# Performance work log

Hardware: AMD Instinct MI355X
Metric: run time of the kernel (lower is better)

## Reference

```python
import math
import jax, jax.numpy as jnp
import numpy as np

B, N, D, H = 4, 2048, 512, 8
HD = D // H


def setup_inputs() -> dict:
    key = jax.random.key(0)
    ks = jax.random.split(key, 7)
    w_scale = 1.0 / math.sqrt(D)  # keep logits in a sane range (like default init)
    return {
        "q": jax.random.normal(ks[0], (B, N, D), dtype=jnp.float32),
        "mask": jax.random.randint(ks[1], (B, N), 0, 2) == 1,  # True = masked key
        "attn_bias": jax.random.normal(ks[2], (B, N, N), dtype=jnp.float32),
        "Wq": jax.random.normal(ks[3], (D, D), dtype=jnp.float32) * w_scale,
        "Wk": jax.random.normal(ks[4], (D, D), dtype=jnp.float32) * w_scale,
        "Wv": jax.random.normal(ks[5], (D, D), dtype=jnp.float32) * w_scale,
        "Wo": jax.random.normal(ks[6], (D, D), dtype=jnp.float32) * w_scale,
    }


def _heads(v):
    # [B, N, D] -> [H, B, N, HD]  (mirrors reshape + movedim(-2, 0))
    b, n, d = v.shape
    return v.reshape(b, n, H, HD).transpose(2, 0, 1, 3)


def reference(q, mask, attn_bias, Wq, Wk, Wv, Wo):
    # Linear projections (torch Linear: x @ W.T)
    qh = _heads(q @ Wq.T)
    kh = _heads(q @ Wk.T)   # self-attention: h defaults to q
    vh = _heads(q @ Wv.T)
    # scores: [H, B, Nq, Nk]
    scores = jnp.einsum("hbqd,hbkd->hbqk", qh, kh) / math.sqrt(HD)
    scores = scores + attn_bias[None]                     # broadcast over heads
    scores = jnp.where(mask[None, :, None, :], -jnp.inf, scores)
    attn = jax.nn.softmax(scores, axis=-1)
    out = jnp.einsum("hbqk,hbkd->hbqd", attn, vh)         # [H, B, Nq, HD]
    out = out.transpose(1, 2, 0, 3).reshape(q.shape[0], q.shape[1], D)
    return out @ Wo.T
```

## Files before the change

kernel.cpp:

```cpp
#include <hip/hip_runtime.h>
#include <stdint.h>


typedef __attribute__((ext_vector_type(8))) short short8;
typedef __attribute__((ext_vector_type(4))) short short4v;
typedef __attribute__((ext_vector_type(4))) float f32x4;

#define DEV static __device__ __forceinline__

constexpr int Bc = 4, Nc = 2048, Dc = 512, Hc = 8, HDc = 64;
constexpr int Mc = Bc * Nc;
constexpr int QKVNc = 3 * Dc;

DEV unsigned short f2bits(float f) {
  union { float f; unsigned u; } a; a.f = f;
  unsigned r = a.u + 0x7fffu + ((a.u >> 16) & 1u);
  return (unsigned short)(r >> 16);
}
DEV unsigned pack_bf16x2(float a, float b) {
  unsigned ua = __float_as_uint(a), ub = __float_as_uint(b);
  ua = ua + 0x7fffu + ((ua >> 16) & 1u);
  ub = ub + 0x7fffu + ((ub >> 16) & 1u);
  return __builtin_amdgcn_perm(ub, ua, 0x07060302);
}
DEV unsigned pack_shorts(short a, short b) {
  return (unsigned)(unsigned short)a | ((unsigned)(unsigned short)b << 16);
}
DEV short8 cvt8(float4 a, float4 b) {
  union { short8 s; uint4 u; } r;
  r.u.x = pack_bf16x2(a.x, a.y); r.u.y = pack_bf16x2(a.z, a.w);
  r.u.z = pack_bf16x2(b.x, b.y); r.u.w = pack_bf16x2(b.z, b.w);
  return r.s;
}

__global__ void cvtw_kernel(const float* __restrict__ Wq, const float* __restrict__ Wk,
                            const float* __restrict__ Wv, const float* __restrict__ Wo,
                            short* __restrict__ Wqkv, short* __restrict__ Wob) {
  int which = blockIdx.x >> 8;
  int j = (blockIdx.x & 255) * 256 + threadIdx.x;
  const float* src = which == 0 ? Wq : which == 1 ? Wk : which == 2 ? Wv : Wo;
  short* dst = (which == 3) ? Wob : Wqkv + which * (Dc * Dc);
  float4 v = ((const float4*)src)[j];
  short4v o = { (short)f2bits(v.x), (short)f2bits(v.y), (short)f2bits(v.z), (short)f2bits(v.w) };
  ((short4v*)dst)[j] = o;
}

__global__ void maskprep_kernel(const void* __restrict__ mask, float* __restrict__ mf) {
  __shared__ int flag;
  if (threadIdx.x == 0) flag = 0;
  __syncthreads();
  const uchar4* m4 = (const uchar4*)mask;
  int acc = 0;
  for (int i = threadIdx.x; i < 2048; i += 1024) {
    uchar4 v = m4[i];
    acc |= (int)v.y | (int)v.z | (int)v.w;
  }
  if (acc) atomicOr(&flag, 1);
  __syncthreads();
  int isbyte = flag;
  for (int i = threadIdx.x; i < Bc * Nc; i += 1024) {
    int v = isbyte ? (int)((const unsigned char*)mask)[i] : ((const int*)mask)[i];
    mf[i] = v ? -1e30f : 0.0f;
  }
}

template<bool A_F32, bool OUT_F32>
__global__ __launch_bounds__(256, 2) void gemm_bt(const void* __restrict__ Av,
                                                  const short* __restrict__ Bm,
                                                  void* __restrict__ Cv,
                                                  int M, int N, int K,
                                                  int qcols, float cscale) {
  __shared__ __align__(16) short At[128 * 72];
  __shared__ __align__(16) short Bt[128 * 72];
  const int tid = threadIdx.x, lane = tid & 63, wv = tid >> 6;
  const int quad = lane >> 4, l16 = lane & 15;
  const int mbase = blockIdx.y * 128, nbase = blockIdx.x * 128;
  const int wr = (wv >> 1) * 64, wc = (wv & 1) * 64;
  const float scale = (nbase < qcols) ? cscale : 1.0f;
  f32x4 acc[4][4] = {};
  float4 apf[4][2]; short8 aph[4], bpre[4];
#pragma unroll
  for (int i = 0; i < 4; i++) {
    int flat = i * 256 + tid, row = flat >> 3, ch8 = (flat & 7) * 8;
    if (A_F32) {
      const float* Af = (const float*)Av;
      apf[i][0] = *(const float4*)&Af[(size_t)(mbase + row) * K + ch8];
      apf[i][1] = *(const float4*)&Af[(size_t)(mbase + row) * K + ch8 + 4];
    } else {
      aph[i] = *(const short8*)&((const short*)Av)[(size_t)(mbase + row) * K + ch8];
    }
    bpre[i] = *(const short8*)&Bm[(size_t)(nbase + row) * K + ch8];
  }
  for (int k0 = 0; k0 < K; k0 += 64) {
    __syncthreads();
#pragma unroll
    for (int i = 0; i < 4; i++) {
      int flat = i * 256 + tid, row = flat >> 3, ch8 = (flat & 7) * 8;
      *(short8*)&At[row * 72 + ch8] = A_F32 ? cvt8(apf[i][0], apf[i][1]) : aph[i];
      *(short8*)&Bt[row * 72 + ch8] = bpre[i];
    }
    if (k0 + 64 < K) {
#pragma unroll
      for (int i = 0; i < 4; i++) {
        int flat = i * 256 + tid, row = flat >> 3, ch8 = (flat & 7) * 8;
        if (A_F32) {
          const float* Af = (const float*)Av;
          apf[i][0] = *(const float4*)&Af[(size_t)(mbase + row) * K + k0 + 64 + ch8];
          apf[i][1] = *(const float4*)&Af[(size_t)(mbase + row) * K + k0 + 64 + ch8 + 4];
        } else {
          aph[i] = *(const short8*)&((const short*)Av)[(size_t)(mbase + row) * K + k0 + 64 + ch8];
        }
        bpre[i] = *(const short8*)&Bm[(size_t)(nbase + row) * K + k0 + 64 + ch8];
      }
    }
    __syncthreads();
#pragma unroll
    for (int s = 0; s < 2; s++) {
      short8 af[4], bf[4];
#pragma unroll
      for (int t = 0; t < 4; t++) {
        af[t] = *(short8*)&At[(wr + t * 16 + l16) * 72 + quad * 8 + s * 32];
        bf[t] = *(short8*)&Bt[(wc + t * 16 + l16) * 72 + quad * 8 + s * 32];
      }
#pragma unroll
      for (int mt = 0; mt < 4; mt++)
#pragma unroll
        for (int nt = 0; nt < 4; nt++)
          acc[mt][nt] = __builtin_amdgcn_mfma_f32_16x16x32_bf16(af[mt], bf[nt], acc[mt][nt], 0, 0, 0);
    }
  }
#pragma unroll
  for (int mt = 0; mt < 4; mt++)
#pragma unroll
    for (int nt = 0; nt < 4; nt++)
#pragma unroll
      for (int r = 0; r < 4; r++) {
        int row = mbase + wr + mt * 16 + quad * 4 + r;
        int col = nbase + wc + nt * 16 + l16;
        float v = acc[mt][nt][r] * scale;
        if (OUT_F32) ((float*)Cv)[(size_t)row * N + col] = v;
        else         ((short*)Cv)[(size_t)row * N + col] = (short)f2bits(v);
      }
}

__global__ __launch_bounds__(512, 3) void attn_kernel(const short* __restrict__ QKV,
                                                      const float* __restrict__ bias,
                                                      const float* __restrict__ maskf,
                                                      short* __restrict__ Aout) {
  __shared__ __align__(16) short Kt[64 * 72];
  __shared__ __align__(16) short Vt[64 * 72];
  __shared__ __align__(16) short Pt[8][16 * 72];
  __shared__ __align__(16) float mlds[Nc];
  __shared__ float lred[8][16];
  const int tid = threadIdx.x, lane = tid & 63, wv = tid >> 6;
  const int quad = lane >> 4, l16 = lane & 15;
  const int qt = blockIdx.x & 15, h = (blockIdx.x >> 4) & 7, b = (int)(blockIdx.x >> 7);
  const int qrow0 = qt * 128;
  const int qglob = qrow0 + wv * 16 + l16;
  const float* biasrow = bias + ((size_t)b * Nc + qglob) * Nc;
  const float* mfb = maskf + b * Nc;

  ((float4*)mlds)[tid] = ((const float4*)mfb)[tid];

  short8 qf[2];
  {
    const short* qp = QKV + (size_t)(b * Nc + qglob) * QKVNc + h * HDc + quad * 8;
    qf[0] = *(const short8*)qp;
    qf[1] = *(const short8*)(qp + 32);
  }

  const int vp = tid & 31, vq = tid >> 5;
  const int krow = tid >> 3, kch = (tid & 7) * 8;
  const short* Kbase = QKV + Dc + h * HDc;
  const short* Vbase = QKV + 2 * Dc + h * HDc;

  short8 kpre; short4v v0pre, v1pre; float4 bpre[4];
  kpre  = *(const short8*)&Kbase[(size_t)(b * Nc + krow) * QKVNc + kch];
  v0pre = *(const short4v*)&Vbase[(size_t)(b * Nc + 2 * vp) * QKVNc + 4 * vq];
  v1pre = *(const short4v*)&Vbase[(size_t)(b * Nc + 2 * vp + 1) * QKVNc + 4 * vq];
#pragma unroll
  for (int t = 0; t < 4; t++) bpre[t] = *(const float4*)&biasrow[t * 16 + quad * 4];

  f32x4 oacc[4] = {};
  float lsum = 0.f;

  for (int kt = 0; kt < 32; kt++) {
    const int kb = kt * 64;
    const int kbn = ((kt + 1) & 31) * 64;
    __syncthreads();
    *(short8*)&Kt[krow * 72 + kch] = kpre;
#pragma unroll
    for (int j = 0; j < 4; j++)
      *(unsigned*)&Vt[(4 * vq + j) * 72 + 2 * vp] = pack_shorts(v0pre[j], v1pre[j]);

    float4 bcur[4];
#pragma unroll
    for (int t = 0; t < 4; t++) bcur[t] = bpre[t];
    kpre  = *(const short8*)&Kbase[(size_t)(b * Nc + kbn + krow) * QKVNc + kch];
    v0pre = *(const short4v*)&Vbase[(size_t)(b * Nc + kbn + 2 * vp) * QKVNc + 4 * vq];
    v1pre = *(const short4v*)&Vbase[(size_t)(b * Nc + kbn + 2 * vp + 1) * QKVNc + 4 * vq];
#pragma unroll
    for (int t = 0; t < 4; t++) bpre[t] = *(const float4*)&biasrow[kbn + t * 16 + quad * 4];
    __syncthreads();

    f32x4 sacc[4] = {};
#pragma unroll
    for (int s = 0; s < 2; s++)
#pragma unroll
      for (int t = 0; t < 4; t++) {
        short8 kf = *(short8*)&Kt[(t * 16 + l16) * 72 + quad * 8 + s * 32];
        sacc[t] = __builtin_amdgcn_mfma_f32_16x16x32_bf16(kf, qf[s], sacc[t], 0, 0, 0);
      }

#pragma unroll
    for (int t = 0; t < 4; t++) {
      float4 mv = *(const float4*)&mlds[kb + t * 16 + quad * 4];
      float p0 = __expf(sacc[t][0] + mv.x + bcur[t].x);
      float p1 = __expf(sacc[t][1] + mv.y + bcur[t].y);
      float p2 = __expf(sacc[t][2] + mv.z + bcur[t].z);
      float p3 = __expf(sacc[t][3] + mv.w + bcur[t].w);
      lsum += (p0 + p1) + (p2 + p3);
      uint2 u = { pack_bf16x2(p0, p1), pack_bf16x2(p2, p3) };
      *(uint2*)&Pt[wv][l16 * 72 + t * 16 + quad * 4] = u;
    }

#pragma unroll
    for (int s = 0; s < 2; s++) {
      short8 pf = *(short8*)&Pt[wv][l16 * 72 + quad * 8 + s * 32];
#pragma unroll
      for (int t = 0; t < 4; t++) {
        short8 vf = *(short8*)&Vt[(t * 16 + l16) * 72 + quad * 8 + s * 32];
        oacc[t] = __builtin_amdgcn_mfma_f32_16x16x32_bf16(pf, vf, oacc[t], 0, 0, 0);
      }
    }
  }

  lsum += __shfl_xor(lsum, 16);
  lsum += __shfl_xor(lsum, 32);
  if (quad == 0) lred[wv][l16] = lsum;
#pragma unroll
  for (int r = 0; r < 4; r++) {
    float inv = 1.0f / lred[wv][quad * 4 + r];
    int row = b * Nc + qrow0 + wv * 16 + quad * 4 + r;
#pragma unroll
    for (int t = 0; t < 4; t++)
      Aout[(size_t)row * Dc + h * HDc + t * 16 + l16] = (short)f2bits(oacc[t][r] * inv);
  }
}

extern "C" void kernel_launch(void* const* d_in, const int* in_sizes, int n_in,
                              void* d_out, int out_size, void* d_ws, size_t ws_size,
                              hipStream_t stream) {
  const float* q    = (const float*)d_in[0];
  const void*  mask = d_in[1];
  const float* bias = (const float*)d_in[2];
  const float* Wq   = (const float*)d_in[3];
  const float* Wk   = (const float*)d_in[4];
  const float* Wv   = (const float*)d_in[5];
  const float* Wo   = (const float*)d_in[6];
  float* out = (float*)d_out;

  char* ws = (char*)d_ws;
  short* Wqkv = (short*)ws;  ws += (size_t)QKVNc * Dc * 2;
  short* Wob  = (short*)ws;  ws += (size_t)Dc * Dc * 2;
  float* mf   = (float*)ws;  ws += (size_t)Bc * Nc * 4;
  short* QKV  = (short*)ws;  ws += (size_t)Mc * QKVNc * 2;
  short* aout = (short*)ws;  ws += (size_t)Mc * Dc * 2;

  cvtw_kernel<<<dim3(1024), dim3(256), 0, stream>>>(Wq, Wk, Wv, Wo, Wqkv, Wob);
  maskprep_kernel<<<dim3(1), dim3(1024), 0, stream>>>(mask, mf);

  gemm_bt<true, false><<<dim3(QKVNc / 128, Mc / 128), dim3(256), 0, stream>>>(
      (const void*)q, Wqkv, (void*)QKV, Mc, QKVNc, Dc, Dc, 0.125f);
  attn_kernel<<<dim3(Bc * Hc * 16), dim3(512), 0, stream>>>(QKV, bias, mf, aout);
  gemm_bt<false, true><<<dim3(Dc / 128, Mc / 128), dim3(256), 0, stream>>>(
      (const void*)aout, Wob, (void*)out, Mc, Dc, Dc, 0, 1.0f);
}
```

Baseline: 261.5 us.

## Use exp2 with prefolded log2e, MFMA row sums, smaller attention blocks

The attention kernel now runs 256-thread blocks over 64 query rows, giving twice as many blocks. Scores come out pre-scaled by log2(e) and are exponentiated with exp2. The bias and mask are preloaded into the MFMA accumulator so the add is folded into the matmul. Row sums of P are computed with an MFMA against a ones vector, which removes the scalar adds and the shuffle reduction. bf16 conversion switches to the native cast, and the new tiling doubles how often each K/V tile is reloaded into LDS across blocks.

```diff
diff --git a/kernel.cpp b/kernel.cpp
--- a/kernel.cpp
+++ b/kernel.cpp
@@ -11,26 +11,31 @@
 constexpr int Bc = 4, Nc = 2048, Dc = 512, Hc = 8, HDc = 64;
 constexpr int Mc = Bc * Nc;
 constexpr int QKVNc = 3 * Dc;
-
-DEV unsigned short f2bits(float f) {
-  union { float f; unsigned u; } a; a.f = f;
-  unsigned r = a.u + 0x7fffu + ((a.u >> 16) & 1u);
-  return (unsigned short)(r >> 16);
-}
-DEV unsigned pack_bf16x2(float a, float b) {
-  unsigned ua = __float_as_uint(a), ub = __float_as_uint(b);
-  ua = ua + 0x7fffu + ((ua >> 16) & 1u);
-  ub = ub + 0x7fffu + ((ub >> 16) & 1u);
-  return __builtin_amdgcn_perm(ub, ua, 0x07060302);
+constexpr float L2E = 1.44269504f;
+
+DEV short bf16cast(float f) {
+  return (short)__builtin_bit_cast(unsigned short, (__bf16)f);
+}
+DEV unsigned cvt_pk_bf16(float a, float b) {
+  unsigned short lb = __builtin_bit_cast(unsigned short, (__bf16)a);
+  unsigned short hb = __builtin_bit_cast(unsigned short, (__bf16)b);
+  return (unsigned)lb | ((unsigned)hb << 16);
 }
 DEV unsigned pack_shorts(short a, short b) {
   return (unsigned)(unsigned short)a | ((unsigned)(unsigned short)b << 16);
 }
 DEV short8 cvt8(float4 a, float4 b) {
   union { short8 s; uint4 u; } r;
-  r.u.x = pack_bf16x2(a.x, a.y); r.u.y = pack_bf16x2(a.z, a.w);
-  r.u.z = pack_bf16x2(b.x, b.y); r.u.w = pack_bf16x2(b.z, b.w);
+  r.u.x = cvt_pk_bf16(a.x, a.y); r.u.y = cvt_pk_bf16(a.z, a.w);
+  r.u.z = cvt_pk_bf16(b.x, b.y); r.u.w = cvt_pk_bf16(b.z, b.w);
   return r.s;
+}
+DEV float fast_exp2(float x) {
+#if __has_builtin(__builtin_amdgcn_exp2f)
+  return __builtin_amdgcn_exp2f(x);
+#else
+  return exp2f(x);
+#endif
 }
 
 __global__ void cvtw_kernel(const float* __restrict__ Wq, const float* __restrict__ Wk,
@@ -41,7 +46,7 @@
   const float* src = which == 0 ? Wq : which == 1 ? Wk : which == 2 ? Wv : Wo;
   short* dst = (which == 3) ? Wob : Wqkv + which * (Dc * Dc);
   float4 v = ((const float4*)src)[j];
-  short4v o = { (short)f2bits(v.x), (short)f2bits(v.y), (short)f2bits(v.z), (short)f2bits(v.w) };
+  short4v o = { bf16cast(v.x), bf16cast(v.y), bf16cast(v.z), bf16cast(v.w) };
   ((short4v*)dst)[j] = o;
 }
 
@@ -139,28 +144,28 @@
         int col = nbase + wc + nt * 16 + l16;
         float v = acc[mt][nt][r] * scale;
         if (OUT_F32) ((float*)Cv)[(size_t)row * N + col] = v;
-        else         ((short*)Cv)[(size_t)row * N + col] = (short)f2bits(v);
-      }
-}
-
-__global__ __launch_bounds__(512, 3) void attn_kernel(const short* __restrict__ QKV,
+        else         ((short*)Cv)[(size_t)row * N + col] = bf16cast(v);
+      }
+}
+
+__global__ __launch_bounds__(256, 4) void attn_kernel(const short* __restrict__ QKV,
                                                       const float* __restrict__ bias,
                                                       const float* __restrict__ maskf,
                                                       short* __restrict__ Aout) {
   __shared__ __align__(16) short Kt[64 * 72];
   __shared__ __align__(16) short Vt[64 * 72];
-  __shared__ __align__(16) short Pt[8][16 * 72];
+  __shared__ __align__(16) short Pt[4][16 * 72];
   __shared__ __align__(16) float mlds[Nc];
-  __shared__ float lred[8][16];
   const int tid = threadIdx.x, lane = tid & 63, wv = tid >> 6;
   const int quad = lane >> 4, l16 = lane & 15;
-  const int qt = blockIdx.x & 15, h = (blockIdx.x >> 4) & 7, b = (int)(blockIdx.x >> 7);
-  const int qrow0 = qt * 128;
+  const int qt = blockIdx.x & 31, h = (blockIdx.x >> 5) & 7, b = (int)(blockIdx.x >> 8);
+  const int qrow0 = qt * 64;
   const int qglob = qrow0 + wv * 16 + l16;
   const float* biasrow = bias + ((size_t)b * Nc + qglob) * Nc;
   const float* mfb = maskf + b * Nc;
 
-  ((float4*)mlds)[tid] = ((const float4*)mfb)[tid];
+  ((float4*)mlds)[tid]       = ((const float4*)mfb)[tid];
+  ((float4*)mlds)[tid + 256] = ((const float4*)mfb)[tid + 256];
 
   short8 qf[2];
   {
@@ -174,36 +179,56 @@
   const short* Kbase = QKV + Dc + h * HDc;
   const short* Vbase = QKV + 2 * Dc + h * HDc;
 
-  short8 kpre; short4v v0pre, v1pre; float4 bpre[4];
-  kpre  = *(const short8*)&Kbase[(size_t)(b * Nc + krow) * QKVNc + kch];
-  v0pre = *(const short4v*)&Vbase[(size_t)(b * Nc + 2 * vp) * QKVNc + 4 * vq];
-  v1pre = *(const short4v*)&Vbase[(size_t)(b * Nc + 2 * vp + 1) * QKVNc + 4 * vq];
+  short8 kpre0, kpre1; short4v v0pre[2], v1pre[2]; float4 bpre[4];
+  kpre0 = *(const short8*)&Kbase[(size_t)(b * Nc + krow) * QKVNc + kch];
+  kpre1 = *(const short8*)&Kbase[(size_t)(b * Nc + krow + 32) * QKVNc + kch];
+#pragma unroll
+  for (int g = 0; g < 2; g++) {
+    v0pre[g] = *(const short4v*)&Vbase[(size_t)(b * Nc + 2 * vp) * QKVNc + 4 * (vq + 8 * g)];
+    v1pre[g] = *(const short4v*)&Vbase[(size_t)(b * Nc + 2 * vp + 1) * QKVNc + 4 * (vq + 8 * g)];
+  }
 #pragma unroll
   for (int t = 0; t < 4; t++) bpre[t] = *(const float4*)&biasrow[t * 16 + quad * 4];
 
+  const short ONEB = (short)0x3F80;
+  const short8 ones = { ONEB, ONEB, ONEB, ONEB, ONEB, ONEB, ONEB, ONEB };
+
   f32x4 oacc[4] = {};
-  float lsum = 0.f;
+  f32x4 sumacc = {};
 
   for (int kt = 0; kt < 32; kt++) {
     const int kb = kt * 64;
     const int kbn = ((kt + 1) & 31) * 64;
     __syncthreads();
-    *(short8*)&Kt[krow * 72 + kch] = kpre;
-#pragma unroll
-    for (int j = 0; j < 4; j++)
-      *(unsigned*)&Vt[(4 * vq + j) * 72 + 2 * vp] = pack_shorts(v0pre[j], v1pre[j]);
-
-    float4 bcur[4];
-#pragma unroll
-    for (int t = 0; t < 4; t++) bcur[t] = bpre[t];
-    kpre  = *(const short8*)&Kbase[(size_t)(b * Nc + kbn + krow) * QKVNc + kch];
-    v0pre = *(const short4v*)&Vbase[(size_t)(b * Nc + kbn + 2 * vp) * QKVNc + 4 * vq];
-    v1pre = *(const short4v*)&Vbase[(size_t)(b * Nc + kbn + 2 * vp + 1) * QKVNc + 4 * vq];
+    *(short8*)&Kt[krow * 72 + kch] = kpre0;
+    *(short8*)&Kt[(krow + 32) * 72 + kch] = kpre1;
+#pragma unroll
+    for (int g = 0; g < 2; g++)
+#pragma unroll
+      for (int j = 0; j < 4; j++)
+        *(unsigned*)&Vt[(4 * (vq + 8 * g) + j) * 72 + 2 * vp] = pack_shorts(v0pre[g][j], v1pre[g][j]);
+
+    f32x4 sacc[4];
+#pragma unroll
+    for (int t = 0; t < 4; t++) {
+      float4 mv = *(const float4*)&mlds[kb + t * 16 + quad * 4];
+      sacc[t][0] = __builtin_fmaf(bpre[t].x, L2E, mv.x);
+      sacc[t][1] = __builtin_fmaf(bpre[t].y, L2E, mv.y);
+      sacc[t][2] = __builtin_fmaf(bpre[t].z, L2E, mv.z);
+      sacc[t][3] = __builtin_fmaf(bpre[t].w, L2E, mv.w);
+    }
+
+    kpre0 = *(const short8*)&Kbase[(size_t)(b * Nc + kbn + krow) * QKVNc + kch];
+    kpre1 = *(const short8*)&Kbase[(size_t)(b * Nc + kbn + krow + 32) * QKVNc + kch];
+#pragma unroll
+    for (int g = 0; g < 2; g++) {
+      v0pre[g] = *(const short4v*)&Vbase[(size_t)(b * Nc + kbn + 2 * vp) * QKVNc + 4 * (vq + 8 * g)];
+      v1pre[g] = *(const short4v*)&Vbase[(size_t)(b * Nc + kbn + 2 * vp + 1) * QKVNc + 4 * (vq + 8 * g)];
+    }
 #pragma unroll
     for (int t = 0; t < 4; t++) bpre[t] = *(const float4*)&biasrow[kbn + t * 16 + quad * 4];
     __syncthreads();
 
-    f32x4 sacc[4] = {};
 #pragma unroll
     for (int s = 0; s < 2; s++)
 #pragma unroll
@@ -214,19 +239,18 @@
 
 #pragma unroll
     for (int t = 0; t < 4; t++) {
-      float4 mv = *(const float4*)&mlds[kb + t * 16 + quad * 4];
-      float p0 = __expf(sacc[t][0] + mv.x + bcur[t].x);
-      float p1 = __expf(sacc[t][1] + mv.y + bcur[t].y);
-      float p2 = __expf(sacc[t][2] + mv.z + bcur[t].z);
-      float p3 = __expf(sacc[t][3] + mv.w + bcur[t].w);
-      lsum += (p0 + p1) + (p2 + p3);
-      uint2 u = { pack_bf16x2(p0, p1), pack_bf16x2(p2, p3) };
+      float p0 = fast_exp2(sacc[t][0]);
+      float p1 = fast_exp2(sacc[t][1]);
+      float p2 = fast_exp2(sacc[t][2]);
+      float p3 = fast_exp2(sacc[t][3]);
+      uint2 u = { cvt_pk_bf16(p0, p1), cvt_pk_bf16(p2, p3) };
       *(uint2*)&Pt[wv][l16 * 72 + t * 16 + quad * 4] = u;
     }
 
 #pragma unroll
     for (int s = 0; s < 2; s++) {
       short8 pf = *(short8*)&Pt[wv][l16 * 72 + quad * 8 + s * 32];
+      sumacc = __builtin_amdgcn_mfma_f32_16x16x32_bf16(pf, ones, sumacc, 0, 0, 0);
 #pragma unroll
       for (int t = 0; t < 4; t++) {
         short8 vf = *(short8*)&Vt[(t * 16 + l16) * 72 + quad * 8 + s * 32];
@@ -235,16 +259,13 @@
     }
   }
 
-  lsum += __shfl_xor(lsum, 16);
-  lsum += __shfl_xor(lsum, 32);
-  if (quad == 0) lred[wv][l16] = lsum;
 #pragma unroll
   for (int r = 0; r < 4; r++) {
-    float inv = 1.0f / lred[wv][quad * 4 + r];
+    float inv = 1.0f / sumacc[r];
     int row = b * Nc + qrow0 + wv * 16 + quad * 4 + r;
 #pragma unroll
     for (int t = 0; t < 4; t++)
-      Aout[(size_t)row * Dc + h * HDc + t * 16 + l16] = (short)f2bits(oacc[t][r] * inv);
+      Aout[(size_t)row * Dc + h * HDc + t * 16 + l16] = bf16cast(oacc[t][r] * inv);
   }
 }
 
@@ -271,8 +292,8 @@
   maskprep_kernel<<<dim3(1), dim3(1024), 0, stream>>>(mask, mf);
 
   gemm_bt<true, false><<<dim3(QKVNc / 128, Mc / 128), dim3(256), 0, stream>>>(
-      (const void*)q, Wqkv, (void*)QKV, Mc, QKVNc, Dc, Dc, 0.125f);
-  attn_kernel<<<dim3(Bc * Hc * 16), dim3(512), 0, stream>>>(QKV, bias, mf, aout);
+      (const void*)q, Wqkv, (void*)QKV, Mc, QKVNc, Dc, Dc, 0.125f * L2E);
+  attn_kernel<<<dim3(Bc * Hc * 32), dim3(256), 0, stream>>>(QKV, bias, mf, aout);
   gemm_bt<false, true><<<dim3(Dc / 128, Mc / 128), dim3(256), 0, stream>>>(
       (const void*)aout, Wob, (void*)out, Mc, Dc, Dc, 0, 1.0f);
 }
```

After: 292.3 us. 1.12x slower.
